# Kernel optimization log

Hardware: AMD Instinct MI355X
Metric: run time of the kernel (lower is better)

Reference implementation:

```python
import jax, jax.numpy as jnp
import numpy as np

B, L, D = 128, 2048, 256
H = 512   # decoder hidden size
U = 256   # attention units

def setup_inputs() -> dict:
    key = jax.random.key(0)
    ks = jax.random.split(key, 8)
    s = lambda fan_in: 1.0 / np.sqrt(fan_in)
    return {
        "features": jax.random.normal(ks[0], (B, L, D), dtype=jnp.float32),
        "hidden": jax.random.normal(ks[1], (B, H), dtype=jnp.float32),
        "W1": jax.random.normal(ks[2], (D, U), dtype=jnp.float32) * s(D),
        "b1": jnp.zeros((U,), dtype=jnp.float32),
        "W2": jax.random.normal(ks[3], (H, U), dtype=jnp.float32) * s(H),
        "b2": jnp.zeros((U,), dtype=jnp.float32),
        "V": jax.random.normal(ks[4], (U, 1), dtype=jnp.float32) * s(U),
        "bV": jnp.zeros((1,), dtype=jnp.float32),
    }

def reference(features, hidden, W1, b1, W2, b2, V, bV):
    # features: [B, L, D], hidden: [B, H]
    proj_f = jnp.einsum('bld,du->blu', features, W1) + b1          # [B, L, U]
    proj_h = (hidden @ W2 + b2)[:, None, :]                         # [B, 1, U]
    score = jnp.tanh(proj_f + proj_h)                               # [B, L, U]
    logits = jnp.einsum('blu,uo->blo', score, V) + bV               # [B, L, 1]
    attention_weights = jax.nn.softmax(logits, axis=1)              # [B, L, 1]
    context_vector = jnp.sum(attention_weights * features, axis=1)  # [B, D]
    return context_vector, attention_weights
```

## Files before the change

kernel.cpp:

```cpp
#include <hip/hip_runtime.h>
#include <hip/hip_bf16.h>

#define B_ 128
#define L_ 2048
#define D_ 256
#define H_ 512
#define U_ 256

typedef _Float16 half8 __attribute__((ext_vector_type(8)));
typedef float f32x4 __attribute__((ext_vector_type(4)));

__device__ __forceinline__ void gll16(const void* gsrc, void* lds) {
  __builtin_amdgcn_global_load_lds(
      (const __attribute__((address_space(1))) unsigned int*)gsrc,
      (__attribute__((address_space(3))) unsigned int*)lds, 16, 0, 0);
}

__global__ __launch_bounds__(256) void kp_w1split(
    const float* __restrict__ W1, _Float16* __restrict__ hi,
    _Float16* __restrict__ lo) {
  int slot = blockIdx.x;
  int u = threadIdx.x;
  union { _Float16 h[8]; float4 f; } H, Lo;
#pragma unroll
  for (int j = 0; j < 8; ++j) {
    float x = W1[(slot * 8 + j) * U_ + u];
    _Float16 h = (_Float16)x;
    H.h[j] = h;
    Lo.h[j] = (_Float16)(x - (float)h);
  }
  *(float4*)&hi[((size_t)slot * U_ + u) * 8] = H.f;
  *(float4*)&lo[((size_t)slot * U_ + u) * 8] = Lo.f;
}

__global__ __launch_bounds__(256) void ka_proj_h(
    const float* __restrict__ hidden, const float* __restrict__ W2,
    const float* __restrict__ b1, const float* __restrict__ b2,
    float* __restrict__ ph) {
  int b = blockIdx.x;
  int u = threadIdx.x;
  __shared__ float hs[H_];
  for (int k = u; k < H_; k += 256) hs[k] = hidden[b * H_ + k];
  __syncthreads();
  float acc = b1[u] + b2[u];
#pragma unroll 8
  for (int k = 0; k < H_; ++k) acc += hs[k] * W2[k * U_ + u];
  ph[b * U_ + u] = acc;
}

#define TLM 64
#define BKC 32
#define NCH (D_ / BKC)

__global__ __launch_bounds__(256, 2) void kb_mfma(
    const float* __restrict__ features, const _Float16* __restrict__ W1s_hi,
    const _Float16* __restrict__ W1s_lo, const float* __restrict__ ph,
    const float* __restrict__ V, float* __restrict__ logits) {
  __shared__ __align__(16) _Float16 Ah[4][TLM][8], Al[4][TLM][8];
  __shared__ __align__(16) _Float16 Bh[2][4][U_][8], Bl[2][4][U_][8];
  __shared__ float red[4][TLM];

  const int tid = threadIdx.x;
  const int w = tid >> 6;
  const int lane = tid & 63;
  const int g = lane >> 4;
  const int c = lane & 15;
  const int b = blockIdx.x >> 5;
  const int l0 = (blockIdx.x & 31) * TLM;
  const int wcol0 = w * 64;
  const float* fbase = features + ((size_t)b * L_ + l0) * D_;

  const int ar = tid & 63;
  const int ag = tid >> 6;
  const float* aptr = fbase + ar * D_ + ag * 8;

  _Float16* bhb[2] = {&Bh[0][0][0][0], &Bh[1][0][0][0]};
  _Float16* blb[2] = {&Bl[0][0][0][0], &Bl[1][0][0][0]};
#define STAGE_B(t, buf)                                                     \
  do {                                                                      \
    const size_t roff = (size_t)(t) * 4 * U_ * 8;          \
    _Pragma("unroll") for (int q = 0; q < 4; ++q) {                         \
      const int poff = (w * 4 + q) * 512;                       \
      gll16(W1s_hi + roff + poff + lane * 8, bhb[buf] + poff);              \
      gll16(W1s_lo + roff + poff + lane * 8, blb[buf] + poff);              \
    }                                                                       \
  } while (0)

#define CONV_WRITE_A(a0, a1)                                                \
  do {                                                                      \
    union { _Float16 h[8]; float4 f; } H, Lo;                               \
    H.h[0] = (_Float16)a0.x; Lo.h[0] = (_Float16)(a0.x - (float)H.h[0]);    \
    H.h[1] = (_Float16)a0.y; Lo.h[1] = (_Float16)(a0.y - (float)H.h[1]);    \
    H.h[2] = (_Float16)a0.z; Lo.h[2] = (_Float16)(a0.z - (float)H.h[2]);    \
    H.h[3] = (_Float16)a0.w; Lo.h[3] = (_Float16)(a0.w - (float)H.h[3]);    \
    H.h[4] = (_Float16)a1.x; Lo.h[4] = (_Float16)(a1.x - (float)H.h[4]);    \
    H.h[5] = (_Float16)a1.y; Lo.h[5] = (_Float16)(a1.y - (float)H.h[5]);    \
    H.h[6] = (_Float16)a1.z; Lo.h[6] = (_Float16)(a1.z - (float)H.h[6]);    \
    H.h[7] = (_Float16)a1.w; Lo.h[7] = (_Float16)(a1.w - (float)H.h[7]);    \
    *(float4*)&Ah[ag][ar][0] = H.f;                                         \
    *(float4*)&Al[ag][ar][0] = Lo.f;                                        \
  } while (0)

  f32x4 acc[4][4];
#pragma unroll
  for (int mt = 0; mt < 4; ++mt)
#pragma unroll
    for (int nt = 0; nt < 4; ++nt) acc[mt][nt] = (f32x4){0.f, 0.f, 0.f, 0.f};

  {
    STAGE_B(0, 0);
    float4 a0 = *(const float4*)(aptr);
    float4 a1 = *(const float4*)(aptr + 4);
    CONV_WRITE_A(a0, a1);
  }
  __syncthreads();

#pragma unroll
  for (int t = 0; t < NCH; ++t) {
    const int buf = t & 1;
    float4 a0, a1;
    if (t < NCH - 1) {
      a0 = *(const float4*)(aptr + (t + 1) * BKC);
      a1 = *(const float4*)(aptr + (t + 1) * BKC + 4);
      STAGE_B(t + 1, buf ^ 1);
    }

    half8 ah[4], al[4], bh[4], bl[4];
#pragma unroll
    for (int mt = 0; mt < 4; ++mt) {
      ah[mt] = *(const half8*)&Ah[g][mt * 16 + c][0];
      al[mt] = *(const half8*)&Al[g][mt * 16 + c][0];
    }
#pragma unroll
    for (int nt = 0; nt < 4; ++nt) {
      bh[nt] = *(const half8*)&Bh[buf][g][wcol0 + nt * 16 + c][0];
      bl[nt] = *(const half8*)&Bl[buf][g][wcol0 + nt * 16 + c][0];
    }
#pragma unroll
    for (int nt = 0; nt < 4; ++nt)
#pragma unroll
      for (int mt = 0; mt < 4; ++mt)
        acc[mt][nt] = __builtin_amdgcn_mfma_f32_16x16x32_f16(ah[mt], bh[nt],
                                                             acc[mt][nt], 0, 0, 0);
#pragma unroll
    for (int nt = 0; nt < 4; ++nt)
#pragma unroll
      for (int mt = 0; mt < 4; ++mt)
        acc[mt][nt] = __builtin_amdgcn_mfma_f32_16x16x32_f16(ah[mt], bl[nt],
                                                             acc[mt][nt], 0, 0, 0);
#pragma unroll
    for (int nt = 0; nt < 4; ++nt)
#pragma unroll
      for (int mt = 0; mt < 4; ++mt)
        acc[mt][nt] = __builtin_amdgcn_mfma_f32_16x16x32_f16(al[mt], bh[nt],
                                                             acc[mt][nt], 0, 0, 0);

    __syncthreads();
    if (t < NCH - 1) {
      CONV_WRITE_A(a0, a1);
      __syncthreads();
    }
  }

  float phv[4], vv[4];
#pragma unroll
  for (int nt = 0; nt < 4; ++nt) {
    int col = wcol0 + nt * 16 + c;
    phv[nt] = ph[b * U_ + col];
    vv[nt] = V[col];
  }
#pragma unroll
  for (int mt = 0; mt < 4; ++mt) {
#pragma unroll
    for (int j = 0; j < 4; ++j) {
      float part = 0.f;
#pragma unroll
      for (int nt = 0; nt < 4; ++nt) {
        float x = acc[mt][nt][j] + phv[nt];
        float e = __expf(2.f * x);
        float tnh = 1.f - 2.f * __builtin_amdgcn_rcpf(e + 1.f);
        part += tnh * vv[nt];
      }
      part += __shfl_xor(part, 1, 16);
      part += __shfl_xor(part, 2, 16);
      part += __shfl_xor(part, 4, 16);
      part += __shfl_xor(part, 8, 16);
      if (c == 0) red[w][mt * 16 + g * 4 + j] = part;
    }
  }
  __syncthreads();
  if (tid < TLM) {
    logits[b * L_ + l0 + tid] =
        red[0][tid] + red[1][tid] + red[2][tid] + red[3][tid];
  }
#undef STAGE_B
#undef CONV_WRITE_A
}

__global__ __launch_bounds__(256) void kc_softmax(
    const float* __restrict__ logits, float* __restrict__ wout) {
  int b = blockIdx.x;
  int tid = threadIdx.x;
  const float* lrow = logits + b * L_;
  float v[8];
  *(float4*)&v[0] = *(const float4*)&lrow[tid * 8];
  *(float4*)&v[4] = *(const float4*)&lrow[tid * 8 + 4];

  float m = v[0];
#pragma unroll
  for (int i = 1; i < 8; ++i) m = fmaxf(m, v[i]);
#pragma unroll
  for (int off = 1; off <= 32; off <<= 1) m = fmaxf(m, __shfl_xor(m, off, 64));
  __shared__ float sm[4];
  if ((tid & 63) == 0) sm[tid >> 6] = m;
  __syncthreads();
  m = fmaxf(fmaxf(sm[0], sm[1]), fmaxf(sm[2], sm[3]));

  float s = 0.f;
#pragma unroll
  for (int i = 0; i < 8; ++i) {
    v[i] = __expf(v[i] - m);
    s += v[i];
  }
#pragma unroll
  for (int off = 1; off <= 32; off <<= 1) s += __shfl_xor(s, off, 64);
  __shared__ float ss[4];
  if ((tid & 63) == 0) ss[tid >> 6] = s;
  __syncthreads();
  s = ss[0] + ss[1] + ss[2] + ss[3];

  float inv = 1.f / s;
#pragma unroll
  for (int i = 0; i < 8; ++i) v[i] *= inv;
  *(float4*)&wout[b * L_ + tid * 8] = *(float4*)&v[0];
  *(float4*)&wout[b * L_ + tid * 8 + 4] = *(float4*)&v[4];
}

__global__ __launch_bounds__(256) void kd_partial(
    const float* __restrict__ features, const float* __restrict__ w,
    float* __restrict__ partials) {
  int bidx = blockIdx.x;
  int b = bidx >> 3;
  int chunk = bidx & 7;
  int tid = threadIdx.x;
  int lq = tid >> 6;
  int dq = tid & 63;
  __shared__ float wsm[256];
  wsm[tid] = w[b * L_ + chunk * 256 + tid];
  __syncthreads();
  const float* fb =
      features + ((size_t)b * L_ + chunk * 256 + lq * 64) * D_ + dq * 4;
  const float* wl = &wsm[lq * 64];
  float4 acc = {0.f, 0.f, 0.f, 0.f};
#pragma unroll 8
  for (int i = 0; i < 64; ++i) {
    float wt = wl[i];
    float4 fv = *(const float4*)(fb + (size_t)i * D_);
    acc.x += wt * fv.x;
    acc.y += wt * fv.y;
    acc.z += wt * fv.z;
    acc.w += wt * fv.w;
  }
  __shared__ float red[4][256];
  *(float4*)&red[lq][dq * 4] = acc;
  __syncthreads();
  float ssum = red[0][tid] + red[1][tid] + red[2][tid] + red[3][tid];
  partials[(size_t)(b * 8 + chunk) * 256 + tid] = ssum;
}

__global__ __launch_bounds__(256) void ke_reduce(
    const float* __restrict__ partials, float* __restrict__ ctx) {
  int b = blockIdx.x;
  int d = threadIdx.x;
  float s = 0.f;
#pragma unroll
  for (int c = 0; c < 8; ++c) s += partials[(size_t)(b * 8 + c) * 256 + d];
  ctx[b * 256 + d] = s;
}

extern "C" void kernel_launch(void* const* d_in, const int* in_sizes, int n_in,
                              void* d_out, int out_size, void* d_ws,
                              size_t ws_size, hipStream_t stream) {
  const float* features = (const float*)d_in[0];
  const float* hidden = (const float*)d_in[1];
  const float* W1 = (const float*)d_in[2];
  const float* b1 = (const float*)d_in[3];
  const float* W2 = (const float*)d_in[4];
  const float* b2 = (const float*)d_in[5];
  const float* V = (const float*)d_in[6];

  float* ws = (float*)d_ws;
  float* ph = ws;
  float* logits = ws + 32768;
  float* partials = ws + 32768 + 262144;
  _Float16* W1s_hi = (_Float16*)(ws + 557056);
  _Float16* W1s_lo = W1s_hi + 65536;

  float* ctx = (float*)d_out;
  float* wout = (float*)d_out + B_ * D_;

  kp_w1split<<<D_ / 8, 256, 0, stream>>>(W1, W1s_hi, W1s_lo);
  ka_proj_h<<<B_, 256, 0, stream>>>(hidden, W2, b1, b2, ph);
  kb_mfma<<<B_ * (L_ / TLM), 256, 0, stream>>>(features, W1s_hi, W1s_lo, ph, V,
                                               logits);
  kc_softmax<<<B_, 256, 0, stream>>>(logits, wout);
  kd_partial<<<B_ * 8, 256, 0, stream>>>(features, wout, partials);
  ke_reduce<<<B_, 256, 0, stream>>>(partials, ctx);
}
```

Baseline: 540.2 us.

## Double MFMA row tile with 512-thread blocks and register-staged single-buffered W1

The projection kernel now processes 128 sequence rows per block using 8 waves in a 2x4 grid, so each W1 chunk staged in LDS is reused across twice as many rows. The asynchronous global-to-LDS double-buffered B staging is replaced by register prefetch and a single LDS buffer, and the reduction scratch is aliased onto the A buffers to keep LDS at 48KB. Launch bounds change to 512 threads with 4 blocks per CU as a target. This roughly halves W1 traffic per row but removes the async copy path and may raise register pressure or lower occupancy.

```diff
diff --git a/kernel.cpp b/kernel.cpp
--- a/kernel.cpp
+++ b/kernel.cpp
@@ -9,12 +9,6 @@
 
 typedef _Float16 half8 __attribute__((ext_vector_type(8)));
 typedef float f32x4 __attribute__((ext_vector_type(4)));
-
-__device__ __forceinline__ void gll16(const void* gsrc, void* lds) {
-  __builtin_amdgcn_global_load_lds(
-      (const __attribute__((address_space(1))) unsigned int*)gsrc,
-      (__attribute__((address_space(3))) unsigned int*)lds, 16, 0, 0);
-}
 
 __global__ __launch_bounds__(256) void kp_w1split(
     const float* __restrict__ W1, _Float16* __restrict__ hi,
@@ -48,57 +42,49 @@
   ph[b * U_ + u] = acc;
 }
 
-#define TLM 64
+#define TLM 128
 #define BKC 32
 #define NCH (D_ / BKC)
 
-__global__ __launch_bounds__(256, 2) void kb_mfma(
+__global__ __launch_bounds__(512, 4) void kb_mfma(
     const float* __restrict__ features, const _Float16* __restrict__ W1s_hi,
     const _Float16* __restrict__ W1s_lo, const float* __restrict__ ph,
     const float* __restrict__ V, float* __restrict__ logits) {
-  __shared__ __align__(16) _Float16 Ah[4][TLM][8], Al[4][TLM][8];
-  __shared__ __align__(16) _Float16 Bh[2][4][U_][8], Bl[2][4][U_][8];
-  __shared__ float red[4][TLM];
+  __shared__ __align__(16) char smem[49152];
+  _Float16(*Ah)[TLM][8] = (_Float16(*)[TLM][8])(smem);
+  _Float16(*Al)[TLM][8] = (_Float16(*)[TLM][8])(smem + 8192);
+  _Float16* Bh = (_Float16*)(smem + 16384);
+  _Float16* Bl = (_Float16*)(smem + 32768);
+  float(*red)[TLM] = (float(*)[TLM])(smem);
 
   const int tid = threadIdx.x;
   const int w = tid >> 6;
   const int lane = tid & 63;
   const int g = lane >> 4;
   const int c = lane & 15;
-  const int b = blockIdx.x >> 5;
-  const int l0 = (blockIdx.x & 31) * TLM;
-  const int wcol0 = w * 64;
+  const int wr = w >> 2;
+  const int wc = w & 3;
+  const int b = blockIdx.x >> 4;
+  const int l0 = (blockIdx.x & 15) * TLM;
   const float* fbase = features + ((size_t)b * L_ + l0) * D_;
 
-  const int ar = tid & 63;
-  const int ag = tid >> 6;
-  const float* aptr = fbase + ar * D_ + ag * 8;
-
-  _Float16* bhb[2] = {&Bh[0][0][0][0], &Bh[1][0][0][0]};
-  _Float16* blb[2] = {&Bl[0][0][0][0], &Bl[1][0][0][0]};
-#define STAGE_B(t, buf)                                                     \
-  do {                                                                      \
-    const size_t roff = (size_t)(t) * 4 * U_ * 8;          \
-    _Pragma("unroll") for (int q = 0; q < 4; ++q) {                         \
-      const int poff = (w * 4 + q) * 512;                       \
-      gll16(W1s_hi + roff + poff + lane * 8, bhb[buf] + poff);              \
-      gll16(W1s_lo + roff + poff + lane * 8, blb[buf] + poff);              \
-    }                                                                       \
-  } while (0)
+  const int ar = tid & 127;
+  const int ag = tid >> 7;
+  const float* aptr = fbase + (size_t)ar * D_ + ag * 8;
 
 #define CONV_WRITE_A(a0, a1)                                                \
   do {                                                                      \
-    union { _Float16 h[8]; float4 f; } H, Lo;                               \
-    H.h[0] = (_Float16)a0.x; Lo.h[0] = (_Float16)(a0.x - (float)H.h[0]);    \
-    H.h[1] = (_Float16)a0.y; Lo.h[1] = (_Float16)(a0.y - (float)H.h[1]);    \
-    H.h[2] = (_Float16)a0.z; Lo.h[2] = (_Float16)(a0.z - (float)H.h[2]);    \
-    H.h[3] = (_Float16)a0.w; Lo.h[3] = (_Float16)(a0.w - (float)H.h[3]);    \
-    H.h[4] = (_Float16)a1.x; Lo.h[4] = (_Float16)(a1.x - (float)H.h[4]);    \
-    H.h[5] = (_Float16)a1.y; Lo.h[5] = (_Float16)(a1.y - (float)H.h[5]);    \
-    H.h[6] = (_Float16)a1.z; Lo.h[6] = (_Float16)(a1.z - (float)H.h[6]);    \
-    H.h[7] = (_Float16)a1.w; Lo.h[7] = (_Float16)(a1.w - (float)H.h[7]);    \
-    *(float4*)&Ah[ag][ar][0] = H.f;                                         \
-    *(float4*)&Al[ag][ar][0] = Lo.f;                                        \
+    union { _Float16 h[8]; float4 f; } Hh, Ll;                              \
+    Hh.h[0] = (_Float16)a0.x; Ll.h[0] = (_Float16)(a0.x - (float)Hh.h[0]);  \
+    Hh.h[1] = (_Float16)a0.y; Ll.h[1] = (_Float16)(a0.y - (float)Hh.h[1]);  \
+    Hh.h[2] = (_Float16)a0.z; Ll.h[2] = (_Float16)(a0.z - (float)Hh.h[2]);  \
+    Hh.h[3] = (_Float16)a0.w; Ll.h[3] = (_Float16)(a0.w - (float)Hh.h[3]);  \
+    Hh.h[4] = (_Float16)a1.x; Ll.h[4] = (_Float16)(a1.x - (float)Hh.h[4]);  \
+    Hh.h[5] = (_Float16)a1.y; Ll.h[5] = (_Float16)(a1.y - (float)Hh.h[5]);  \
+    Hh.h[6] = (_Float16)a1.z; Ll.h[6] = (_Float16)(a1.z - (float)Hh.h[6]);  \
+    Hh.h[7] = (_Float16)a1.w; Ll.h[7] = (_Float16)(a1.w - (float)Hh.h[7]);  \
+    *(float4*)&Ah[ag][ar][0] = Hh.f;                                        \
+    *(float4*)&Al[ag][ar][0] = Ll.f;                                        \
   } while (0)
 
   f32x4 acc[4][4];
@@ -108,33 +94,44 @@
     for (int nt = 0; nt < 4; ++nt) acc[mt][nt] = (f32x4){0.f, 0.f, 0.f, 0.f};
 
   {
-    STAGE_B(0, 0);
     float4 a0 = *(const float4*)(aptr);
     float4 a1 = *(const float4*)(aptr + 4);
+    float4 h0 = *(const float4*)&W1s_hi[(size_t)tid * 8];
+    float4 h1 = *(const float4*)&W1s_hi[(size_t)(tid + 512) * 8];
+    float4 q0 = *(const float4*)&W1s_lo[(size_t)tid * 8];
+    float4 q1 = *(const float4*)&W1s_lo[(size_t)(tid + 512) * 8];
     CONV_WRITE_A(a0, a1);
+    *(float4*)&Bh[(size_t)tid * 8] = h0;
+    *(float4*)&Bh[(size_t)(tid + 512) * 8] = h1;
+    *(float4*)&Bl[(size_t)tid * 8] = q0;
+    *(float4*)&Bl[(size_t)(tid + 512) * 8] = q1;
   }
   __syncthreads();
 
 #pragma unroll
   for (int t = 0; t < NCH; ++t) {
-    const int buf = t & 1;
-    float4 a0, a1;
+    float4 a0, a1, h0, h1, q0, q1;
     if (t < NCH - 1) {
+      const size_t roff = (size_t)(t + 1) * 8192;
       a0 = *(const float4*)(aptr + (t + 1) * BKC);
       a1 = *(const float4*)(aptr + (t + 1) * BKC + 4);
-      STAGE_B(t + 1, buf ^ 1);
+      h0 = *(const float4*)&W1s_hi[roff + (size_t)tid * 8];
+      h1 = *(const float4*)&W1s_hi[roff + (size_t)(tid + 512) * 8];
+      q0 = *(const float4*)&W1s_lo[roff + (size_t)tid * 8];
+      q1 = *(const float4*)&W1s_lo[roff + (size_t)(tid + 512) * 8];
     }
 
     half8 ah[4], al[4], bh[4], bl[4];
 #pragma unroll
     for (int mt = 0; mt < 4; ++mt) {
-      ah[mt] = *(const half8*)&Ah[g][mt * 16 + c][0];
-      al[mt] = *(const half8*)&Al[g][mt * 16 + c][0];
+      ah[mt] = *(const half8*)&Ah[g][wr * 64 + mt * 16 + c][0];
+      al[mt] = *(const half8*)&Al[g][wr * 64 + mt * 16 + c][0];
     }
 #pragma unroll
     for (int nt = 0; nt < 4; ++nt) {
-      bh[nt] = *(const half8*)&Bh[buf][g][wcol0 + nt * 16 + c][0];
-      bl[nt] = *(const half8*)&Bl[buf][g][wcol0 + nt * 16 + c][0];
+      const int u = wc * 64 + nt * 16 + c;
+      bh[nt] = *(const half8*)&Bh[((size_t)g * U_ + u) * 8];
+      bl[nt] = *(const half8*)&Bl[((size_t)g * U_ + u) * 8];
     }
 #pragma unroll
     for (int nt = 0; nt < 4; ++nt)
@@ -158,6 +155,10 @@
     __syncthreads();
     if (t < NCH - 1) {
       CONV_WRITE_A(a0, a1);
+      *(float4*)&Bh[(size_t)tid * 8] = h0;
+      *(float4*)&Bh[(size_t)(tid + 512) * 8] = h1;
+      *(float4*)&Bl[(size_t)tid * 8] = q0;
+      *(float4*)&Bl[(size_t)(tid + 512) * 8] = q1;
       __syncthreads();
     }
   }
@@ -165,7 +166,7 @@
   float phv[4], vv[4];
 #pragma unroll
   for (int nt = 0; nt < 4; ++nt) {
-    int col = wcol0 + nt * 16 + c;
+    int col = wc * 64 + nt * 16 + c;
     phv[nt] = ph[b * U_ + col];
     vv[nt] = V[col];
   }
@@ -185,7 +186,7 @@
       part += __shfl_xor(part, 2, 16);
       part += __shfl_xor(part, 4, 16);
       part += __shfl_xor(part, 8, 16);
-      if (c == 0) red[w][mt * 16 + g * 4 + j] = part;
+      if (c == 0) red[wc][wr * 64 + mt * 16 + g * 4 + j] = part;
     }
   }
   __syncthreads();
@@ -193,7 +194,6 @@
     logits[b * L_ + l0 + tid] =
         red[0][tid] + red[1][tid] + red[2][tid] + red[3][tid];
   }
-#undef STAGE_B
 #undef CONV_WRITE_A
 }
 
@@ -301,7 +301,7 @@
 
   kp_w1split<<<D_ / 8, 256, 0, stream>>>(W1, W1s_hi, W1s_lo);
   ka_proj_h<<<B_, 256, 0, stream>>>(hidden, W2, b1, b2, ph);
-  kb_mfma<<<B_ * (L_ / TLM), 256, 0, stream>>>(features, W1s_hi, W1s_lo, ph, V,
+  kb_mfma<<<B_ * (L_ / TLM), 512, 0, stream>>>(features, W1s_hi, W1s_lo, ph, V,
                                                logits);
   kc_softmax<<<B_, 256, 0, stream>>>(logits, wout);
   kd_partial<<<B_ * 8, 256, 0, stream>>>(features, wout, partials);
```

Result: faster. 487.1 us (-9.8%).
